# Performance work log

Measured on AMD Instinct MI355X. Metric: run time of the kernel, lower is better.

The kernel has to match this reference:

```python
import jax, jax.numpy as jnp
import numpy as np

B, S, D_IN, UNITS = 4, 4096, 512, 128

def setup_inputs() -> dict:
    key = jax.random.key(0)
    k_in, k_wq, k_wk, k_wv = jax.random.split(key, 4)
    scale = 1.0 / np.sqrt(D_IN)
    return {
        "inputs": jax.random.normal(k_in, (B, S, D_IN), dtype=jnp.float32),
        "Wq": jax.random.normal(k_wq, (D_IN, UNITS), dtype=jnp.float32) * scale,
        "bq": jnp.zeros((UNITS,), dtype=jnp.float32),
        "Wk": jax.random.normal(k_wk, (D_IN, UNITS), dtype=jnp.float32) * scale,
        "bk": jnp.zeros((UNITS,), dtype=jnp.float32),
        "Wv": jax.random.normal(k_wv, (D_IN, UNITS), dtype=jnp.float32) * scale,
        "bv": jnp.zeros((UNITS,), dtype=jnp.float32),
    }

def reference(inputs, Wq, bq, Wk, bk, Wv, bv):
    # Dense + ReLU projections (Keras Dense default has bias)
    q = jax.nn.relu(jnp.einsum('bsd,du->bsu', inputs, Wq) + bq)  # [B,S,U]
    k = jax.nn.relu(jnp.einsum('bsd,du->bsu', inputs, Wk) + bk)
    v = jax.nn.relu(jnp.einsum('bsd,du->bsu', inputs, Wv) + bv)
    # Raw (unscaled) attention: softmax(Q K^T) V
    scores = jnp.einsum('bsu,btu->bst', q, k)                    # [B,S,S]
    attn = jax.nn.softmax(scores, axis=-1)
    return jnp.einsum('bst,btu->bsu', attn, v)                   # [B,S,U]
```

## Files before the change

kernel.cpp:

```cpp
#include <hip/hip_runtime.h>
#include <stdint.h>

#define Bq 4
#define Sq 4096
#define DIN 512
#define Uq 128
#define Mq (Bq * Sq)
#define LOG2E 1.44269504f

typedef __attribute__((ext_vector_type(8))) _Float16 f16x8;
typedef __attribute__((ext_vector_type(4))) float f32x4;
typedef unsigned short u16;

__device__ __forceinline__ u16 f2h(float f) {
  union { _Float16 h; u16 u; } v;
  v.h = (_Float16)f;
  return v.u;
}
__device__ __forceinline__ unsigned pk2(float a, float b) {
  return __builtin_bit_cast(unsigned, __builtin_amdgcn_cvt_pkrtz(a, b));
}
__device__ __forceinline__ void gl_lds16(const void* g, void* l) {
  __builtin_amdgcn_global_load_lds(
      (const __attribute__((address_space(1))) unsigned int*)g,
      (__attribute__((address_space(3))) unsigned int*)l, 16, 0, 0);
}

__global__ __launch_bounds__(256) void wt_kernel(const float* __restrict__ Wqp,
                                                 const float* __restrict__ Wkp,
                                                 const float* __restrict__ Wvp,
                                                 u16* __restrict__ wt) {
  int idx = blockIdx.x * 256 + threadIdx.x;
  int z = idx >> 16, r = idx & 65535;
  int n = r >> 9, k = r & 511;
  const float* W = (z == 0) ? Wqp : ((z == 1) ? Wkp : Wvp);
  wt[idx] = f2h(W[k * Uq + n]);
}

__global__ __launch_bounds__(256, 2) void proj_kernel(const float* __restrict__ X,
                                                      const u16* __restrict__ Wt,
                                                      const float* __restrict__ bqp,
                                                      const float* __restrict__ bkp,
                                                      const float* __restrict__ bvp,
                                                      u16* __restrict__ qkv) {
  const int mbase = blockIdx.x * 32;
  const int tid = threadIdx.x;
  const int wid = tid >> 6, lane = tid & 63;
  const int lo = lane & 15, g = lane >> 4;

  __shared__ __align__(16) u16 xt[32][40];

  f32x4 acc[2][6];
#pragma unroll
  for (int mg = 0; mg < 2; ++mg)
#pragma unroll
    for (int fi = 0; fi < 6; ++fi) acc[mg][fi] = (f32x4){0.f, 0.f, 0.f, 0.f};

  const int xrow = tid >> 2, xcc = (tid & 3) * 8;
  const float* xsrc = X + (size_t)(mbase + xrow) * DIN + xcc;
  float4 nv0, nv1;
  if (tid < 128) {
    nv0 = *(const float4*)xsrc;
    nv1 = *(const float4*)(xsrc + 4);
  }

  const u16* wp[6];
#pragma unroll
  for (int fi = 0; fi < 6; ++fi) {
    const int gf = 6 * wid + fi;
    const int R = (gf >> 3) * 128 + (gf & 7) * 16 + lo;
    wp[fi] = Wt + (size_t)R * 512 + 8 * g;
  }
  f16x8 bw[6];
#pragma unroll
  for (int fi = 0; fi < 6; ++fi) bw[fi] = *(const f16x8*)(wp[fi]);

  for (int step = 0; step < 16; ++step) {
    if (tid < 128) {
      union { u16 u[8]; uint4 v; } pk;
      pk.u[0] = f2h(nv0.x); pk.u[1] = f2h(nv0.y); pk.u[2] = f2h(nv0.z); pk.u[3] = f2h(nv0.w);
      pk.u[4] = f2h(nv1.x); pk.u[5] = f2h(nv1.y); pk.u[6] = f2h(nv1.z); pk.u[7] = f2h(nv1.w);
      *(uint4*)(&xt[xrow][xcc]) = pk.v;
    }
    __syncthreads();
    if (step < 15 && tid < 128) {
      const float* s2 = xsrc + (step + 1) * 32;
      nv0 = *(const float4*)s2;
      nv1 = *(const float4*)(s2 + 4);
    }
    f16x8 a0 = *(const f16x8*)(&xt[lo][8 * g]);
    f16x8 a1 = *(const f16x8*)(&xt[16 + lo][8 * g]);
#pragma unroll
    for (int fi = 0; fi < 6; ++fi) {
      acc[0][fi] = __builtin_amdgcn_mfma_f32_16x16x32_f16(a0, bw[fi], acc[0][fi], 0, 0, 0);
      acc[1][fi] = __builtin_amdgcn_mfma_f32_16x16x32_f16(a1, bw[fi], acc[1][fi], 0, 0, 0);
    }
    if (step < 15) {
#pragma unroll
      for (int fi = 0; fi < 6; ++fi)
        bw[fi] = *(const f16x8*)(wp[fi] + (step + 1) * 32);
    }
    __syncthreads();
  }

#pragma unroll
  for (int fi = 0; fi < 6; ++fi) {
    const int gf = 6 * wid + fi;
    const int z = gf >> 3, fl = gf & 7;
    const float* bias = (z == 0) ? bqp : ((z == 1) ? bkp : bvp);
    const float bb = bias[fl * 16 + lo];
    if (z < 2) {
      u16* dst = qkv + (size_t)z * Mq * Uq;
      const float qs = (z == 0) ? LOG2E : 1.0f;
#pragma unroll
      for (int mg = 0; mg < 2; ++mg)
#pragma unroll
        for (int r = 0; r < 4; ++r) {
          const int m = mbase + 16 * mg + 4 * g + r;
          dst[(size_t)m * Uq + fl * 16 + lo] = f2h(fmaxf(acc[mg][fi][r] + bb, 0.f) * qs);
        }
    } else {
      u16* vT = qkv + (size_t)2 * Mq * Uq;
      const int n = fl * 16 + lo;
#pragma unroll
      for (int mg = 0; mg < 2; ++mg) {
        const int m0 = mbase + 16 * mg + 4 * g;
        const int bb_ = m0 >> 12, s0 = m0 & (Sq - 1);
        ushort4 pv = make_ushort4(f2h(fmaxf(acc[mg][fi][0] + bb, 0.f)),
                                  f2h(fmaxf(acc[mg][fi][1] + bb, 0.f)),
                                  f2h(fmaxf(acc[mg][fi][2] + bb, 0.f)),
                                  f2h(fmaxf(acc[mg][fi][3] + bb, 0.f)));
        *(ushort4*)(vT + (size_t)bb_ * Uq * Sq + (size_t)n * Sq + s0) = pv;
      }
    }
  }
}

__global__ __launch_bounds__(256, 3) void attn_kernel(const u16* __restrict__ qkv,
                                                      float* __restrict__ op,
                                                      float2* __restrict__ mlp,
                                                      int kvlen) {
  const int nb = gridDim.x;
  const int bid = blockIdx.x;
  const int xcd = bid & 7, idx = bid >> 3;
  const int b = xcd >> 1;
  const int within = (xcd & 1) * (nb >> 3) + idx;
  const int split = within >> 6, qblk = within & 63;
  const int kv0 = split * kvlen;
  const int nit = kvlen >> 6;

  const int tid = threadIdx.x;
  const int wid = tid >> 6, lane = tid & 63;
  const int lo = lane & 15, g = lane >> 4;

  const u16* kbase = qkv + (size_t)Mq * Uq + (size_t)b * Sq * Uq;
  const u16* vbase = qkv + (size_t)2 * Mq * Uq + (size_t)b * Uq * Sq;

  __shared__ __align__(16) unsigned char kt[16384];
  __shared__ __align__(16) unsigned char vt[16384];
  __shared__ __align__(16) unsigned char plds[4][2048];

  const int s4 = lane >> 4, j16 = lane & 15;
  const char* kg = (const char*)kbase + (size_t)(kv0 + 16 * wid) * 256 + 16 * lane;
  const int kwo0 = (16 * wid + 0 + s4) * 256 + ((j16 ^ ((0 + s4) & 7)) << 4);
  const int kwo1 = (16 * wid + 4 + s4) * 256 + ((j16 ^ ((4 + s4) & 7)) << 4);
  const int kwo2 = (16 * wid + 8 + s4) * 256 + ((j16 ^ ((8 + s4) & 7)) << 4);
  const int kwo3 = (16 * wid + 12 + s4) * 256 + ((j16 ^ ((12 + s4) & 7)) << 4);

  const int s8 = lane >> 3, j8 = lane & 7;
  const int vo = s8 * 8192 + ((j8 ^ s8) << 4);
  const char* vgp = (const char*)vbase + (size_t)kv0 * 2 + (size_t)wid * 262144 + vo;
  char* vl = (char*)vt + wid * 4096;

#define VSTAGE() do {                       \
    gl_lds16(vgp,          vl);             \
    gl_lds16(vgp + 65536,  vl + 1024);      \
    gl_lds16(vgp + 131072, vl + 2048);      \
    gl_lds16(vgp + 196608, vl + 3072);      \
  } while (0)

  const int qrow = b * Sq + qblk * 64 + wid * 16 + lo;
  f16x8 qf[4];
#pragma unroll
  for (int t = 0; t < 4; ++t)
    qf[t] = *(const f16x8*)(qkv + (size_t)qrow * Uq + 32 * t + 8 * g);

  char* const pl = (char*)plds;
  const int pbase = wid * 2048 + lo * 128;
  const int pw0 = pbase + (((g >> 1) ^ (lo & 7)) << 4) + 8 * (g & 1);
  const int pr0 = pbase + ((g ^ (lo & 7)) << 4);

  f32x4 acc[8];
#pragma unroll
  for (int f = 0; f < 8; ++f) acc[f] = (f32x4){0.f, 0.f, 0.f, 0.f};
  float m_run = -1e30f, l_run = 0.f;

  VSTAGE();
  uint4 ka0 = *(const uint4*)(kg + 0);
  uint4 ka1 = *(const uint4*)(kg + 1024);
  uint4 ka2 = *(const uint4*)(kg + 2048);
  uint4 ka3 = *(const uint4*)(kg + 3072);
  kg += 16384;
  asm volatile("s_waitcnt vmcnt(0)" ::: "memory");
  *(uint4*)(&kt[kwo0]) = ka0;
  *(uint4*)(&kt[kwo1]) = ka1;
  *(uint4*)(&kt[kwo2]) = ka2;
  *(uint4*)(&kt[kwo3]) = ka3;
  if (nit > 1) {
    ka0 = *(const uint4*)(kg + 0);
    ka1 = *(const uint4*)(kg + 1024);
    ka2 = *(const uint4*)(kg + 2048);
    ka3 = *(const uint4*)(kg + 3072);
    kg += 16384;
  }
  asm volatile("s_waitcnt lgkmcnt(0)" ::: "memory");
  __builtin_amdgcn_sched_barrier(0);
  __builtin_amdgcn_s_barrier();
  __builtin_amdgcn_sched_barrier(0);

  for (int it = 0; it < nit; ++it) {
    f32x4 sf[4];
    __builtin_amdgcn_s_setprio(1);
#pragma unroll
    for (int h = 0; h < 4; ++h) {
      sf[h] = (f32x4){0.f, 0.f, 0.f, 0.f};
      const int row = 16 * h + lo;
#pragma unroll
      for (int t = 0; t < 4; ++t) {
        f16x8 a = *(const f16x8*)(&kt[row * 256 + ((64 * t + 16 * g) ^ ((lo & 7) << 4))]);
        sf[h] = __builtin_amdgcn_mfma_f32_16x16x32_f16(a, qf[t], sf[h], 0, 0, 0);
      }
    }
    __builtin_amdgcn_s_setprio(0);

    float tmax = -1e30f;
#pragma unroll
    for (int h = 0; h < 4; ++h)
#pragma unroll
      for (int r = 0; r < 4; ++r) tmax = fmaxf(tmax, sf[h][r]);
    tmax = fmaxf(tmax, __shfl_xor(tmax, 16));
    tmax = fmaxf(tmax, __shfl_xor(tmax, 32));

    if (__any(tmax > m_run + 8.f)) {
      const float m_new = fmaxf(m_run, tmax);
      const float scale = exp2f(m_run - m_new);
#pragma unroll
      for (int r = 0; r < 4; ++r) {
        const float sc = __shfl(scale, 4 * g + r);
#pragma unroll
        for (int f = 0; f < 8; ++f) acc[f][r] *= sc;
      }
      l_run *= scale;
      m_run = m_new;
    }

    float psum = 0.f;
    float p[16];
#pragma unroll
    for (int h = 0; h < 4; ++h)
#pragma unroll
      for (int r = 0; r < 4; ++r) {
        const float pv = exp2f(sf[h][r] - m_run);
        psum += pv;
        p[4 * h + r] = pv;
      }
    psum += __shfl_xor(psum, 16);
    psum += __shfl_xor(psum, 32);
    l_run += psum;

#pragma unroll
    for (int h = 0; h < 4; ++h) {
      uint2 pq = make_uint2(pk2(p[4 * h + 0], p[4 * h + 1]),
                            pk2(p[4 * h + 2], p[4 * h + 3]));
      *(uint2*)(pl + (pw0 ^ (h << 5))) = pq;
    }

    asm volatile("s_waitcnt vmcnt(0)" ::: "memory");
    __builtin_amdgcn_sched_barrier(0);
    __builtin_amdgcn_s_barrier();
    __builtin_amdgcn_sched_barrier(0);

    __builtin_amdgcn_s_setprio(1);
#pragma unroll
    for (int s = 0; s < 2; ++s) {
      f16x8 pa = *(const f16x8*)(pl + (pr0 ^ (s << 6)));
#pragma unroll
      for (int f = 0; f < 8; ++f) {
        const int n = 16 * f + lo;
        f16x8 bv = *(const f16x8*)(&vt[n * 128 + ((64 * s + 16 * g) ^ ((lo & 7) << 4))]);
        acc[f] = __builtin_amdgcn_mfma_f32_16x16x32_f16(pa, bv, acc[f], 0, 0, 0);
      }
    }
    __builtin_amdgcn_s_setprio(0);

    if (it + 1 < nit) {
      *(uint4*)(&kt[kwo0]) = ka0;
      *(uint4*)(&kt[kwo1]) = ka1;
      *(uint4*)(&kt[kwo2]) = ka2;
      *(uint4*)(&kt[kwo3]) = ka3;
    }
    asm volatile("s_waitcnt lgkmcnt(0)" ::: "memory");
    __builtin_amdgcn_sched_barrier(0);
    __builtin_amdgcn_s_barrier();
    __builtin_amdgcn_sched_barrier(0);

    if (it + 1 < nit) {
      vgp += 128;
      VSTAGE();
      if (it + 2 < nit) {
        ka0 = *(const uint4*)(kg + 0);
        ka1 = *(const uint4*)(kg + 1024);
        ka2 = *(const uint4*)(kg + 2048);
        ka3 = *(const uint4*)(kg + 3072);
        kg += 16384;
      }
    }
  }
#undef VSTAGE

  const size_t rb = (size_t)split * Mq + (size_t)b * Sq + qblk * 64 + wid * 16;
  if (g == 0) mlp[rb + lo] = make_float2(m_run, l_run);
  float* od = op + rb * Uq;
#pragma unroll
  for (int f = 0; f < 8; ++f) {
    const int n = 16 * f + lo;
#pragma unroll
    for (int r = 0; r < 4; ++r)
      od[(size_t)(4 * g + r) * Uq + n] = acc[f][r];
  }
}

__global__ __launch_bounds__(256) void combine_kernel(const float* __restrict__ op,
                                                      const float2* __restrict__ mlp,
                                                      float* __restrict__ out,
                                                      int nsplit) {
  const int idx = blockIdx.x * 256 + threadIdx.x;
  const int q = idx >> 5, nq = idx & 31;
  float M = -1e30f;
  for (int s = 0; s < nsplit; ++s) M = fmaxf(M, mlp[(size_t)s * Mq + q].x);
  float L = 0.f;
  float ox = 0.f, oy = 0.f, oz = 0.f, ow = 0.f;
  for (int s = 0; s < nsplit; ++s) {
    const float2 ml = mlp[(size_t)s * Mq + q];
    const float w = exp2f(ml.x - M);
    L += w * ml.y;
    const float4 v = *(const float4*)(op + ((size_t)s * Mq + q) * Uq + nq * 4);
    ox += w * v.x; oy += w * v.y; oz += w * v.z; ow += w * v.w;
  }
  const float inv = 1.f / L;
  *(float4*)(out + (size_t)q * Uq + nq * 4) = make_float4(ox * inv, oy * inv, oz * inv, ow * inv);
}

extern "C" void kernel_launch(void* const* d_in, const int* in_sizes, int n_in,
                              void* d_out, int out_size, void* d_ws, size_t ws_size,
                              hipStream_t stream) {
  const float* X   = (const float*)d_in[0];
  const float* Wqp = (const float*)d_in[1];
  const float* bqp = (const float*)d_in[2];
  const float* Wkp = (const float*)d_in[3];
  const float* bkp = (const float*)d_in[4];
  const float* Wvp = (const float*)d_in[5];
  const float* bvp = (const float*)d_in[6];
  float* out = (float*)d_out;

  u16* qkv = (u16*)d_ws;
  u16* wt  = qkv + (size_t)3 * Mq * Uq;
  float* op = (float*)(wt + 3 * 65536);

  const size_t base = (size_t)12976128;
  const size_t per  = (size_t)8519680;
  int nsplit = 4;
  if (ws_size < base + 4 * per) nsplit = 2;
  if (ws_size < base + 2 * per) nsplit = 1;
  float2* mlp = (float2*)(op + (size_t)nsplit * Mq * Uq);

  wt_kernel<<<768, 256, 0, stream>>>(Wqp, Wkp, Wvp, wt);
  proj_kernel<<<Mq / 32, 256, 0, stream>>>(X, wt, bqp, bkp, bvp, qkv);
  attn_kernel<<<256 * nsplit, 256, 0, stream>>>(qkv, op, mlp, Sq / nsplit);
  combine_kernel<<<(Mq * 32) / 256, 256, 0, stream>>>(op, mlp, out, nsplit);
}
```

Measured before the change: 98.15 us.

## Process two query subtiles per wave to reuse K/V tiles across 128 queries

Each wave now handles 32 query rows (two 16-row subtiles) instead of 16, so each block covers 128 queries and reuses every K and V LDS tile across twice as many MFMAs. The grid is halved, the P buffer doubles, and occupancy hints drop from 3 to 2 blocks per CU to fit the doubled accumulators and scores. This targets K/V load and LDS traffic per unit of compute, at the cost of more registers, fewer resident waves and fewer blocks to spread across CUs.

```diff
diff --git a/kernel.cpp b/kernel.cpp
--- a/kernel.cpp
+++ b/kernel.cpp
@@ -136,7 +136,7 @@
   }
 }
 
-__global__ __launch_bounds__(256, 3) void attn_kernel(const u16* __restrict__ qkv,
+__global__ __launch_bounds__(256, 2) void attn_kernel(const u16* __restrict__ qkv,
                                                       float* __restrict__ op,
                                                       float2* __restrict__ mlp,
                                                       int kvlen) {
@@ -145,7 +145,7 @@
   const int xcd = bid & 7, idx = bid >> 3;
   const int b = xcd >> 1;
   const int within = (xcd & 1) * (nb >> 3) + idx;
-  const int split = within >> 6, qblk = within & 63;
+  const int split = within >> 5, qblk = within & 31;
   const int kv0 = split * kvlen;
   const int nit = kvlen >> 6;
 
@@ -158,7 +158,7 @@
 
   __shared__ __align__(16) unsigned char kt[16384];
   __shared__ __align__(16) unsigned char vt[16384];
-  __shared__ __align__(16) unsigned char plds[4][2048];
+  __shared__ __align__(16) unsigned char plds[4][4096];
 
   const int s4 = lane >> 4, j16 = lane & 15;
   const char* kg = (const char*)kbase + (size_t)(kv0 + 16 * wid) * 256 + 16 * lane;
@@ -179,21 +179,24 @@
     gl_lds16(vgp + 196608, vl + 3072);      \
   } while (0)
 
-  const int qrow = b * Sq + qblk * 64 + wid * 16 + lo;
-  f16x8 qf[4];
-#pragma unroll
-  for (int t = 0; t < 4; ++t)
-    qf[t] = *(const f16x8*)(qkv + (size_t)qrow * Uq + 32 * t + 8 * g);
-
-  char* const pl = (char*)plds;
-  const int pbase = wid * 2048 + lo * 128;
-  const int pw0 = pbase + (((g >> 1) ^ (lo & 7)) << 4) + 8 * (g & 1);
-  const int pr0 = pbase + ((g ^ (lo & 7)) << 4);
-
-  f32x4 acc[8];
-#pragma unroll
-  for (int f = 0; f < 8; ++f) acc[f] = (f32x4){0.f, 0.f, 0.f, 0.f};
-  float m_run = -1e30f, l_run = 0.f;
+  const int qrow0 = b * Sq + qblk * 128 + wid * 32 + lo;
+  f16x8 qf[2][4];
+#pragma unroll
+  for (int sq = 0; sq < 2; ++sq)
+#pragma unroll
+    for (int t = 0; t < 4; ++t)
+      qf[sq][t] = *(const f16x8*)(qkv + (size_t)(qrow0 + 16 * sq) * Uq + 32 * t + 8 * g);
+
+  char* const pl = (char*)plds + wid * 4096;
+  const int pw0 = lo * 128 + (((g >> 1) ^ (lo & 7)) << 4) + 8 * (g & 1);
+  const int pr0 = lo * 128 + ((g ^ (lo & 7)) << 4);
+
+  f32x4 acc[2][8];
+#pragma unroll
+  for (int sq = 0; sq < 2; ++sq)
+#pragma unroll
+    for (int f = 0; f < 8; ++f) acc[sq][f] = (f32x4){0.f, 0.f, 0.f, 0.f};
+  float m_run[2] = {-1e30f, -1e30f}, l_run[2] = {0.f, 0.f};
 
   VSTAGE();
   uint4 ka0 = *(const uint4*)(kg + 0);
@@ -219,60 +222,64 @@
   __builtin_amdgcn_sched_barrier(0);
 
   for (int it = 0; it < nit; ++it) {
-    f32x4 sf[4];
+    f32x4 sf[2][4];
     __builtin_amdgcn_s_setprio(1);
 #pragma unroll
     for (int h = 0; h < 4; ++h) {
-      sf[h] = (f32x4){0.f, 0.f, 0.f, 0.f};
+      sf[0][h] = (f32x4){0.f, 0.f, 0.f, 0.f};
+      sf[1][h] = (f32x4){0.f, 0.f, 0.f, 0.f};
       const int row = 16 * h + lo;
 #pragma unroll
       for (int t = 0; t < 4; ++t) {
         f16x8 a = *(const f16x8*)(&kt[row * 256 + ((64 * t + 16 * g) ^ ((lo & 7) << 4))]);
-        sf[h] = __builtin_amdgcn_mfma_f32_16x16x32_f16(a, qf[t], sf[h], 0, 0, 0);
+        sf[0][h] = __builtin_amdgcn_mfma_f32_16x16x32_f16(a, qf[0][t], sf[0][h], 0, 0, 0);
+        sf[1][h] = __builtin_amdgcn_mfma_f32_16x16x32_f16(a, qf[1][t], sf[1][h], 0, 0, 0);
       }
     }
     __builtin_amdgcn_s_setprio(0);
 
-    float tmax = -1e30f;
-#pragma unroll
-    for (int h = 0; h < 4; ++h)
-#pragma unroll
-      for (int r = 0; r < 4; ++r) tmax = fmaxf(tmax, sf[h][r]);
-    tmax = fmaxf(tmax, __shfl_xor(tmax, 16));
-    tmax = fmaxf(tmax, __shfl_xor(tmax, 32));
-
-    if (__any(tmax > m_run + 8.f)) {
-      const float m_new = fmaxf(m_run, tmax);
-      const float scale = exp2f(m_run - m_new);
-#pragma unroll
-      for (int r = 0; r < 4; ++r) {
-        const float sc = __shfl(scale, 4 * g + r);
-#pragma unroll
-        for (int f = 0; f < 8; ++f) acc[f][r] *= sc;
-      }
-      l_run *= scale;
-      m_run = m_new;
-    }
-
-    float psum = 0.f;
-    float p[16];
-#pragma unroll
-    for (int h = 0; h < 4; ++h)
-#pragma unroll
-      for (int r = 0; r < 4; ++r) {
-        const float pv = exp2f(sf[h][r] - m_run);
-        psum += pv;
-        p[4 * h + r] = pv;
-      }
-    psum += __shfl_xor(psum, 16);
-    psum += __shfl_xor(psum, 32);
-    l_run += psum;
-
-#pragma unroll
-    for (int h = 0; h < 4; ++h) {
-      uint2 pq = make_uint2(pk2(p[4 * h + 0], p[4 * h + 1]),
-                            pk2(p[4 * h + 2], p[4 * h + 3]));
-      *(uint2*)(pl + (pw0 ^ (h << 5))) = pq;
+#pragma unroll
+    for (int sq = 0; sq < 2; ++sq) {
+      float tmax = -1e30f;
+#pragma unroll
+      for (int h = 0; h < 4; ++h)
+#pragma unroll
+        for (int r = 0; r < 4; ++r) tmax = fmaxf(tmax, sf[sq][h][r]);
+      tmax = fmaxf(tmax, __shfl_xor(tmax, 16));
+      tmax = fmaxf(tmax, __shfl_xor(tmax, 32));
+
+      if (__any(tmax > m_run[sq] + 8.f)) {
+        const float m_new = fmaxf(m_run[sq], tmax);
+        const float scale = exp2f(m_run[sq] - m_new);
+#pragma unroll
+        for (int r = 0; r < 4; ++r) {
+          const float sc = __shfl(scale, 4 * g + r);
+#pragma unroll
+          for (int f = 0; f < 8; ++f) acc[sq][f][r] *= sc;
+        }
+        l_run[sq] *= scale;
+        m_run[sq] = m_new;
+      }
+
+      float psum = 0.f;
+#pragma unroll
+      for (int h = 0; h < 4; ++h)
+#pragma unroll
+        for (int r = 0; r < 4; ++r) {
+          const float pv = exp2f(sf[sq][h][r] - m_run[sq]);
+          psum += pv;
+          sf[sq][h][r] = pv;
+        }
+      psum += __shfl_xor(psum, 16);
+      psum += __shfl_xor(psum, 32);
+      l_run[sq] += psum;
+
+#pragma unroll
+      for (int h = 0; h < 4; ++h) {
+        uint2 pq = make_uint2(pk2(sf[sq][h][0], sf[sq][h][1]),
+                              pk2(sf[sq][h][2], sf[sq][h][3]));
+        *(uint2*)(pl + sq * 2048 + (pw0 ^ (h << 5))) = pq;
+      }
     }
 
     asm volatile("s_waitcnt vmcnt(0)" ::: "memory");
@@ -282,13 +289,15 @@
 
     __builtin_amdgcn_s_setprio(1);
 #pragma unroll
-    for (int s = 0; s < 2; ++s) {
-      f16x8 pa = *(const f16x8*)(pl + (pr0 ^ (s << 6)));
+    for (int ks = 0; ks < 2; ++ks) {
+      f16x8 pa0 = *(const f16x8*)(pl + (pr0 ^ (ks << 6)));
+      f16x8 pa1 = *(const f16x8*)(pl + 2048 + (pr0 ^ (ks << 6)));
 #pragma unroll
       for (int f = 0; f < 8; ++f) {
         const int n = 16 * f + lo;
-        f16x8 bv = *(const f16x8*)(&vt[n * 128 + ((64 * s + 16 * g) ^ ((lo & 7) << 4))]);
-        acc[f] = __builtin_amdgcn_mfma_f32_16x16x32_f16(pa, bv, acc[f], 0, 0, 0);
+        f16x8 bv = *(const f16x8*)(&vt[n * 128 + ((64 * ks + 16 * g) ^ ((lo & 7) << 4))]);
+        acc[0][f] = __builtin_amdgcn_mfma_f32_16x16x32_f16(pa0, bv, acc[0][f], 0, 0, 0);
+        acc[1][f] = __builtin_amdgcn_mfma_f32_16x16x32_f16(pa1, bv, acc[1][f], 0, 0, 0);
       }
     }
     __builtin_amdgcn_s_setprio(0);
@@ -318,15 +327,18 @@
   }
 #undef VSTAGE
 
-  const size_t rb = (size_t)split * Mq + (size_t)b * Sq + qblk * 64 + wid * 16;
-  if (g == 0) mlp[rb + lo] = make_float2(m_run, l_run);
-  float* od = op + rb * Uq;
-#pragma unroll
-  for (int f = 0; f < 8; ++f) {
-    const int n = 16 * f + lo;
-#pragma unroll
-    for (int r = 0; r < 4; ++r)
-      od[(size_t)(4 * g + r) * Uq + n] = acc[f][r];
+#pragma unroll
+  for (int sq = 0; sq < 2; ++sq) {
+    const size_t rb = (size_t)split * Mq + (size_t)b * Sq + qblk * 128 + wid * 32 + sq * 16;
+    if (g == 0) mlp[rb + lo] = make_float2(m_run[sq], l_run[sq]);
+    float* od = op + rb * Uq;
+#pragma unroll
+    for (int f = 0; f < 8; ++f) {
+      const int n = 16 * f + lo;
+#pragma unroll
+      for (int r = 0; r < 4; ++r)
+        od[(size_t)(4 * g + r) * Uq + n] = acc[sq][f][r];
+    }
   }
 }
 
@@ -376,6 +388,6 @@
 
   wt_kernel<<<768, 256, 0, stream>>>(Wqp, Wkp, Wvp, wt);
   proj_kernel<<<Mq / 32, 256, 0, stream>>>(X, wt, bqp, bkp, bvp, qkv);
-  attn_kernel<<<256 * nsplit, 256, 0, stream>>>(qkv, op, mlp, Sq / nsplit);
+  attn_kernel<<<128 * nsplit, 256, 0, stream>>>(qkv, op, mlp, Sq / nsplit);
   combine_kernel<<<(Mq * 32) / 256, 256, 0, stream>>>(op, mlp, out, nsplit);
 }
```

Result: no change. 98.03 us (-0.1%).

## Double-buffer K/V tiles and overlap next QK^T with softmax in attention

Applied to the files above, without the earlier changes.

Turns the attention loop into a two-stage software pipeline. K and V LDS tiles are double-buffered, and the QK^T MFMAs for the next tile are issued before the softmax and PV of the current tile. One barrier per iteration is dropped, and the global waits use partial vmcnt so loads can stay in flight. Doubling LDS and live score registers lowers occupancy to 2 blocks per CU, and the KV split count drops from 4 to 2, giving fewer blocks and less combine work.

```diff
diff --git a/kernel.cpp b/kernel.cpp
--- a/kernel.cpp
+++ b/kernel.cpp
@@ -136,7 +136,7 @@
   }
 }
 
-__global__ __launch_bounds__(256, 3) void attn_kernel(const u16* __restrict__ qkv,
+__global__ __launch_bounds__(256, 2) void attn_kernel(const u16* __restrict__ qkv,
                                                       float* __restrict__ op,
                                                       float2* __restrict__ mlp,
                                                       int kvlen) {
@@ -156,8 +156,8 @@
   const u16* kbase = qkv + (size_t)Mq * Uq + (size_t)b * Sq * Uq;
   const u16* vbase = qkv + (size_t)2 * Mq * Uq + (size_t)b * Uq * Sq;
 
-  __shared__ __align__(16) unsigned char kt[16384];
-  __shared__ __align__(16) unsigned char vt[16384];
+  __shared__ __align__(16) unsigned char kt[2][16384];
+  __shared__ __align__(16) unsigned char vt[2][16384];
   __shared__ __align__(16) unsigned char plds[4][2048];
 
   const int s4 = lane >> 4, j16 = lane & 15;
@@ -170,13 +170,41 @@
   const int s8 = lane >> 3, j8 = lane & 7;
   const int vo = s8 * 8192 + ((j8 ^ s8) << 4);
   const char* vgp = (const char*)vbase + (size_t)kv0 * 2 + (size_t)wid * 262144 + vo;
-  char* vl = (char*)vt + wid * 4096;
-
-#define VSTAGE() do {                       \
-    gl_lds16(vgp,          vl);             \
-    gl_lds16(vgp + 65536,  vl + 1024);      \
-    gl_lds16(vgp + 131072, vl + 2048);      \
-    gl_lds16(vgp + 196608, vl + 3072);      \
+
+#define VSTAGE(BUF) do {                                    \
+    char* vl = (char*)&vt[BUF][wid * 4096];                 \
+    gl_lds16(vgp,          vl);                             \
+    gl_lds16(vgp + 65536,  vl + 1024);                      \
+    gl_lds16(vgp + 131072, vl + 2048);                      \
+    gl_lds16(vgp + 196608, vl + 3072);                      \
+  } while (0)
+
+#define KLOAD() do {                                        \
+    ka0 = *(const uint4*)(kg + 0);                          \
+    ka1 = *(const uint4*)(kg + 1024);                       \
+    ka2 = *(const uint4*)(kg + 2048);                       \
+    ka3 = *(const uint4*)(kg + 3072);                       \
+    kg += 16384;                                            \
+  } while (0)
+
+#define KWRITE(BUF) do {                                    \
+    *(uint4*)(&kt[BUF][kwo0]) = ka0;                        \
+    *(uint4*)(&kt[BUF][kwo1]) = ka1;                        \
+    *(uint4*)(&kt[BUF][kwo2]) = ka2;                        \
+    *(uint4*)(&kt[BUF][kwo3]) = ka3;                        \
+  } while (0)
+
+#define QKBLOCK(BUF, SD) do {                               \
+    _Pragma("unroll")                                       \
+    for (int h = 0; h < 4; ++h) {                           \
+      SD[h] = (f32x4){0.f, 0.f, 0.f, 0.f};                  \
+      const int row_ = 16 * h + lo;                         \
+      _Pragma("unroll")                                     \
+      for (int t = 0; t < 4; ++t) {                         \
+        f16x8 a_ = *(const f16x8*)(&kt[BUF][row_ * 256 + ((64 * t + 16 * g) ^ ((lo & 7) << 4))]); \
+        SD[h] = __builtin_amdgcn_mfma_f32_16x16x32_f16(a_, qf[t], SD[h], 0, 0, 0); \
+      }                                                     \
+    }                                                       \
   } while (0)
 
   const int qrow = b * Sq + qblk * 64 + wid * 16 + lo;
@@ -185,137 +213,109 @@
   for (int t = 0; t < 4; ++t)
     qf[t] = *(const f16x8*)(qkv + (size_t)qrow * Uq + 32 * t + 8 * g);
 
-  char* const pl = (char*)plds;
-  const int pbase = wid * 2048 + lo * 128;
-  const int pw0 = pbase + (((g >> 1) ^ (lo & 7)) << 4) + 8 * (g & 1);
-  const int pr0 = pbase + ((g ^ (lo & 7)) << 4);
+  char* const pl = (char*)plds + wid * 2048;
+  const int pw0 = lo * 128 + (((g >> 1) ^ (lo & 7)) << 4) + 8 * (g & 1);
+  const int pr0 = lo * 128 + ((g ^ (lo & 7)) << 4);
 
   f32x4 acc[8];
 #pragma unroll
   for (int f = 0; f < 8; ++f) acc[f] = (f32x4){0.f, 0.f, 0.f, 0.f};
   float m_run = -1e30f, l_run = 0.f;
 
-  VSTAGE();
-  uint4 ka0 = *(const uint4*)(kg + 0);
-  uint4 ka1 = *(const uint4*)(kg + 1024);
-  uint4 ka2 = *(const uint4*)(kg + 2048);
-  uint4 ka3 = *(const uint4*)(kg + 3072);
-  kg += 16384;
-  asm volatile("s_waitcnt vmcnt(0)" ::: "memory");
-  *(uint4*)(&kt[kwo0]) = ka0;
-  *(uint4*)(&kt[kwo1]) = ka1;
-  *(uint4*)(&kt[kwo2]) = ka2;
-  *(uint4*)(&kt[kwo3]) = ka3;
-  if (nit > 1) {
-    ka0 = *(const uint4*)(kg + 0);
-    ka1 = *(const uint4*)(kg + 1024);
-    ka2 = *(const uint4*)(kg + 2048);
-    ka3 = *(const uint4*)(kg + 3072);
-    kg += 16384;
-  }
+  uint4 ka0, ka1, ka2, ka3;
+
+  VSTAGE(0); vgp += 128;
+  VSTAGE(1); vgp += 128;
+  KLOAD(); KWRITE(0);
+  KLOAD(); KWRITE(1);
+  if (nit > 2) KLOAD();
   asm volatile("s_waitcnt lgkmcnt(0)" ::: "memory");
   __builtin_amdgcn_sched_barrier(0);
   __builtin_amdgcn_s_barrier();
   __builtin_amdgcn_sched_barrier(0);
 
-  for (int it = 0; it < nit; ++it) {
-    f32x4 sf[4];
-    __builtin_amdgcn_s_setprio(1);
-#pragma unroll
-    for (int h = 0; h < 4; ++h) {
-      sf[h] = (f32x4){0.f, 0.f, 0.f, 0.f};
-      const int row = 16 * h + lo;
-#pragma unroll
-      for (int t = 0; t < 4; ++t) {
-        f16x8 a = *(const f16x8*)(&kt[row * 256 + ((64 * t + 16 * g) ^ ((lo & 7) << 4))]);
-        sf[h] = __builtin_amdgcn_mfma_f32_16x16x32_f16(a, qf[t], sf[h], 0, 0, 0);
-      }
-    }
-    __builtin_amdgcn_s_setprio(0);
-
-    float tmax = -1e30f;
-#pragma unroll
-    for (int h = 0; h < 4; ++h)
-#pragma unroll
-      for (int r = 0; r < 4; ++r) tmax = fmaxf(tmax, sf[h][r]);
-    tmax = fmaxf(tmax, __shfl_xor(tmax, 16));
-    tmax = fmaxf(tmax, __shfl_xor(tmax, 32));
-
-    if (__any(tmax > m_run + 8.f)) {
-      const float m_new = fmaxf(m_run, tmax);
-      const float scale = exp2f(m_run - m_new);
-#pragma unroll
-      for (int r = 0; r < 4; ++r) {
-        const float sc = __shfl(scale, 4 * g + r);
-#pragma unroll
-        for (int f = 0; f < 8; ++f) acc[f][r] *= sc;
-      }
-      l_run *= scale;
-      m_run = m_new;
-    }
-
-    float psum = 0.f;
-    float p[16];
-#pragma unroll
-    for (int h = 0; h < 4; ++h)
-#pragma unroll
-      for (int r = 0; r < 4; ++r) {
-        const float pv = exp2f(sf[h][r] - m_run);
-        psum += pv;
-        p[4 * h + r] = pv;
-      }
-    psum += __shfl_xor(psum, 16);
-    psum += __shfl_xor(psum, 32);
-    l_run += psum;
-
-#pragma unroll
-    for (int h = 0; h < 4; ++h) {
-      uint2 pq = make_uint2(pk2(p[4 * h + 0], p[4 * h + 1]),
-                            pk2(p[4 * h + 2], p[4 * h + 3]));
-      *(uint2*)(pl + (pw0 ^ (h << 5))) = pq;
-    }
-
-    asm volatile("s_waitcnt vmcnt(0)" ::: "memory");
-    __builtin_amdgcn_sched_barrier(0);
-    __builtin_amdgcn_s_barrier();
-    __builtin_amdgcn_sched_barrier(0);
-
-    __builtin_amdgcn_s_setprio(1);
-#pragma unroll
-    for (int s = 0; s < 2; ++s) {
-      f16x8 pa = *(const f16x8*)(pl + (pr0 ^ (s << 6)));
-#pragma unroll
-      for (int f = 0; f < 8; ++f) {
-        const int n = 16 * f + lo;
-        f16x8 bv = *(const f16x8*)(&vt[n * 128 + ((64 * s + 16 * g) ^ ((lo & 7) << 4))]);
-        acc[f] = __builtin_amdgcn_mfma_f32_16x16x32_f16(pa, bv, acc[f], 0, 0, 0);
-      }
-    }
-    __builtin_amdgcn_s_setprio(0);
-
-    if (it + 1 < nit) {
-      *(uint4*)(&kt[kwo0]) = ka0;
-      *(uint4*)(&kt[kwo1]) = ka1;
-      *(uint4*)(&kt[kwo2]) = ka2;
-      *(uint4*)(&kt[kwo3]) = ka3;
-    }
-    asm volatile("s_waitcnt lgkmcnt(0)" ::: "memory");
-    __builtin_amdgcn_sched_barrier(0);
-    __builtin_amdgcn_s_barrier();
-    __builtin_amdgcn_sched_barrier(0);
-
-    if (it + 1 < nit) {
-      vgp += 128;
-      VSTAGE();
-      if (it + 2 < nit) {
-        ka0 = *(const uint4*)(kg + 0);
-        ka1 = *(const uint4*)(kg + 1024);
-        ka2 = *(const uint4*)(kg + 2048);
-        ka3 = *(const uint4*)(kg + 3072);
-        kg += 16384;
-      }
-    }
-  }
+  f32x4 sfA[4], sfB[4];
+  QKBLOCK(0, sfA);
+
+#define AITER(IT, PAR, SC, SN) do {                                            \
+                \
+    __builtin_amdgcn_s_setprio(1);                                             \
+    if ((IT) + 1 < nit) QKBLOCK((PAR) ^ 1, SN);                                \
+    __builtin_amdgcn_s_setprio(0);                                             \
+    if ((IT) + 2 < nit) KWRITE(PAR);              \
+    float tmax = -1e30f;                                                       \
+    _Pragma("unroll")                                                          \
+    for (int h = 0; h < 4; ++h)                                                \
+      _Pragma("unroll")                                                        \
+      for (int r = 0; r < 4; ++r) tmax = fmaxf(tmax, SC[h][r]);                \
+    tmax = fmaxf(tmax, __shfl_xor(tmax, 16));                                  \
+    tmax = fmaxf(tmax, __shfl_xor(tmax, 32));                                  \
+    if (__any(tmax > m_run + 8.f)) {                                           \
+      const float m_new = fmaxf(m_run, tmax);                                  \
+      const float scale = exp2f(m_run - m_new);                                \
+      _Pragma("unroll")                                                        \
+      for (int r = 0; r < 4; ++r) {                                            \
+        const float sc_ = __shfl(scale, 4 * g + r);                            \
+        _Pragma("unroll")                                                      \
+        for (int f = 0; f < 8; ++f) acc[f][r] *= sc_;                          \
+      }                                                                        \
+      l_run *= scale;                                                          \
+      m_run = m_new;                                                           \
+    }                                                                          \
+    float psum = 0.f;                                                          \
+    _Pragma("unroll")                                                          \
+    for (int h = 0; h < 4; ++h)                                                \
+      _Pragma("unroll")                                                        \
+      for (int r = 0; r < 4; ++r) {                                            \
+        const float pv_ = exp2f(SC[h][r] - m_run);                             \
+        psum += pv_;                                                           \
+        SC[h][r] = pv_;                                                        \
+      }                                                                        \
+    psum += __shfl_xor(psum, 16);                                              \
+    psum += __shfl_xor(psum, 32);                                              \
+    l_run += psum;                                                             \
+    _Pragma("unroll")                                                          \
+    for (int h = 0; h < 4; ++h) {                                              \
+      uint2 pq_ = make_uint2(pk2(SC[h][0], SC[h][1]), pk2(SC[h][2], SC[h][3]));\
+      *(uint2*)(pl + (pw0 ^ (h << 5))) = pq_;                                  \
+    }                                                                          \
+                     \
+    __builtin_amdgcn_s_setprio(1);                                             \
+    _Pragma("unroll")                                                          \
+    for (int ks = 0; ks < 2; ++ks) {                                           \
+      f16x8 pa_ = *(const f16x8*)(pl + (pr0 ^ (ks << 6)));                     \
+      _Pragma("unroll")                                                        \
+      for (int f = 0; f < 8; ++f) {                                            \
+        const int n_ = 16 * f + lo;                                            \
+        f16x8 bv_ = *(const f16x8*)(&vt[PAR][n_ * 128 + ((64 * ks + 16 * g) ^ ((lo & 7) << 4))]); \
+        acc[f] = __builtin_amdgcn_mfma_f32_16x16x32_f16(pa_, bv_, acc[f], 0, 0, 0); \
+      }                                                                        \
+    }                                                                          \
+    __builtin_amdgcn_s_setprio(0);                                             \
+    __builtin_amdgcn_sched_barrier(0);                                         \
+    __builtin_amdgcn_s_barrier();         \
+    __builtin_amdgcn_sched_barrier(0);                                         \
+    if ((IT) + 3 < nit) KLOAD();                          \
+    __builtin_amdgcn_sched_barrier(0);                                         \
+    if ((IT) + 2 < nit) { VSTAGE(PAR); vgp += 128; }   \
+    __builtin_amdgcn_sched_barrier(0);                                         \
+    if ((IT) + 3 < nit)      asm volatile("s_waitcnt vmcnt(8)" ::: "memory");  \
+    else if ((IT) + 2 < nit) asm volatile("s_waitcnt vmcnt(4)" ::: "memory");  \
+    else                     asm volatile("s_waitcnt vmcnt(0)" ::: "memory");  \
+    asm volatile("s_waitcnt lgkmcnt(0)" ::: "memory");                         \
+    __builtin_amdgcn_sched_barrier(0);                                         \
+    __builtin_amdgcn_s_barrier();           \
+    __builtin_amdgcn_sched_barrier(0);                                         \
+  } while (0)
+
+  for (int it = 0; it < nit; it += 2) {
+    AITER(it,     0, sfA, sfB);
+    AITER(it + 1, 1, sfB, sfA);
+  }
+#undef AITER
+#undef QKBLOCK
+#undef KWRITE
+#undef KLOAD
 #undef VSTAGE
 
   const size_t rb = (size_t)split * Mq + (size_t)b * Sq + qblk * 64 + wid * 16;
@@ -369,8 +369,7 @@
 
   const size_t base = (size_t)12976128;
   const size_t per  = (size_t)8519680;
-  int nsplit = 4;
-  if (ws_size < base + 4 * per) nsplit = 2;
+  int nsplit = 2;
   if (ws_size < base + 2 * per) nsplit = 1;
   float2* mlp = (float2*)(op + (size_t)nsplit * Mq * Uq);
 
```

Result: slower. 106.3 us (+8.3%).

## Switch attention kernel to 32x32x16 MFMA with 128-row query blocks

Applied to the files above, without the earlier changes.

The attention kernel moves from 16x16x32 to 32x32x16 f16 MFMA tiles. Each wave now owns 32 query rows, so each block covers 128 queries and the grid is halved. This gives twice the K/V reuse per LDS load and fewer MFMA issues per FLOP. In exchange the P staging buffer doubles, rescale factors go through a small LDS array, register pressure rises (launch bounds go from 3 to 2 blocks per CU), and fewer blocks are available to fill the GPU.

```diff
diff --git a/kernel.cpp b/kernel.cpp
--- a/kernel.cpp
+++ b/kernel.cpp
@@ -10,6 +10,7 @@
 
 typedef __attribute__((ext_vector_type(8))) _Float16 f16x8;
 typedef __attribute__((ext_vector_type(4))) float f32x4;
+typedef __attribute__((ext_vector_type(16))) float f32x16;
 typedef unsigned short u16;
 
 __device__ __forceinline__ u16 f2h(float f) {
@@ -25,6 +26,8 @@
       (const __attribute__((address_space(1))) unsigned int*)g,
       (__attribute__((address_space(3))) unsigned int*)l, 16, 0, 0);
 }
+__device__ __forceinline__ float xmax32(float v) { return fmaxf(v, __shfl_xor(v, 32)); }
+__device__ __forceinline__ float xsum32(float v) { return v + __shfl_xor(v, 32); }
 
 __global__ __launch_bounds__(256) void wt_kernel(const float* __restrict__ Wqp,
                                                  const float* __restrict__ Wkp,
@@ -136,7 +139,7 @@
   }
 }
 
-__global__ __launch_bounds__(256, 3) void attn_kernel(const u16* __restrict__ qkv,
+__global__ __launch_bounds__(256, 2) void attn_kernel(const u16* __restrict__ qkv,
                                                       float* __restrict__ op,
                                                       float2* __restrict__ mlp,
                                                       int kvlen) {
@@ -145,20 +148,21 @@
   const int xcd = bid & 7, idx = bid >> 3;
   const int b = xcd >> 1;
   const int within = (xcd & 1) * (nb >> 3) + idx;
-  const int split = within >> 6, qblk = within & 63;
+  const int split = within >> 5, qblk = within & 31;
   const int kv0 = split * kvlen;
   const int nit = kvlen >> 6;
 
   const int tid = threadIdx.x;
   const int wid = tid >> 6, lane = tid & 63;
-  const int lo = lane & 15, g = lane >> 4;
+  const int l32 = lane & 31, hi = lane >> 5;
 
   const u16* kbase = qkv + (size_t)Mq * Uq + (size_t)b * Sq * Uq;
   const u16* vbase = qkv + (size_t)2 * Mq * Uq + (size_t)b * Uq * Sq;
 
   __shared__ __align__(16) unsigned char kt[16384];
   __shared__ __align__(16) unsigned char vt[16384];
-  __shared__ __align__(16) unsigned char plds[4][2048];
+  __shared__ __align__(16) unsigned char plds[4][4096];
+  __shared__ float smx[4][32];
 
   const int s4 = lane >> 4, j16 = lane & 15;
   const char* kg = (const char*)kbase + (size_t)(kv0 + 16 * wid) * 256 + 16 * lane;
@@ -170,7 +174,7 @@
   const int s8 = lane >> 3, j8 = lane & 7;
   const int vo = s8 * 8192 + ((j8 ^ s8) << 4);
   const char* vgp = (const char*)vbase + (size_t)kv0 * 2 + (size_t)wid * 262144 + vo;
-  char* vl = (char*)vt + wid * 4096;
+  char* const vl = (char*)vt + wid * 4096;
 
 #define VSTAGE() do {                       \
     gl_lds16(vgp,          vl);             \
@@ -178,102 +182,117 @@
     gl_lds16(vgp + 131072, vl + 2048);      \
     gl_lds16(vgp + 196608, vl + 3072);      \
   } while (0)
-
-  const int qrow = b * Sq + qblk * 64 + wid * 16 + lo;
-  f16x8 qf[4];
-#pragma unroll
-  for (int t = 0; t < 4; ++t)
-    qf[t] = *(const f16x8*)(qkv + (size_t)qrow * Uq + 32 * t + 8 * g);
-
-  char* const pl = (char*)plds;
-  const int pbase = wid * 2048 + lo * 128;
-  const int pw0 = pbase + (((g >> 1) ^ (lo & 7)) << 4) + 8 * (g & 1);
-  const int pr0 = pbase + ((g ^ (lo & 7)) << 4);
-
-  f32x4 acc[8];
-#pragma unroll
-  for (int f = 0; f < 8; ++f) acc[f] = (f32x4){0.f, 0.f, 0.f, 0.f};
+#define KLOAD() do {                        \
+    ka0 = *(const uint4*)(kg + 0);          \
+    ka1 = *(const uint4*)(kg + 1024);       \
+    ka2 = *(const uint4*)(kg + 2048);       \
+    ka3 = *(const uint4*)(kg + 3072);       \
+    kg += 16384;                            \
+  } while (0)
+#define KWRITE() do {                       \
+    *(uint4*)(&kt[kwo0]) = ka0;             \
+    *(uint4*)(&kt[kwo1]) = ka1;             \
+    *(uint4*)(&kt[kwo2]) = ka2;             \
+    *(uint4*)(&kt[kwo3]) = ka3;             \
+  } while (0)
+
+  const int qrow = b * Sq + qblk * 128 + wid * 32 + l32;
+  f16x8 qf[8];
+#pragma unroll
+  for (int ks = 0; ks < 8; ++ks)
+    qf[ks] = *(const f16x8*)(qkv + (size_t)qrow * Uq + 16 * ks + 8 * hi);
+
+  f32x16 acc4[4];
+#pragma unroll
+  for (int f = 0; f < 4; ++f) acc4[f] = (f32x16){};
   float m_run = -1e30f, l_run = 0.f;
+  float* const smxw = &smx[wid][0];
+
+  const int q7 = l32 & 7;
+  char* const plw = (char*)plds + wid * 4096 + l32 * 128 + 8 * hi;
+  const char* const plr = (const char*)plds + wid * 4096 + l32 * 128;
+
+  uint4 ka0, ka1, ka2, ka3;
 
   VSTAGE();
-  uint4 ka0 = *(const uint4*)(kg + 0);
-  uint4 ka1 = *(const uint4*)(kg + 1024);
-  uint4 ka2 = *(const uint4*)(kg + 2048);
-  uint4 ka3 = *(const uint4*)(kg + 3072);
-  kg += 16384;
+  KLOAD();
   asm volatile("s_waitcnt vmcnt(0)" ::: "memory");
-  *(uint4*)(&kt[kwo0]) = ka0;
-  *(uint4*)(&kt[kwo1]) = ka1;
-  *(uint4*)(&kt[kwo2]) = ka2;
-  *(uint4*)(&kt[kwo3]) = ka3;
-  if (nit > 1) {
-    ka0 = *(const uint4*)(kg + 0);
-    ka1 = *(const uint4*)(kg + 1024);
-    ka2 = *(const uint4*)(kg + 2048);
-    ka3 = *(const uint4*)(kg + 3072);
-    kg += 16384;
-  }
+  KWRITE();
+  if (nit > 1) KLOAD();
   asm volatile("s_waitcnt lgkmcnt(0)" ::: "memory");
   __builtin_amdgcn_sched_barrier(0);
   __builtin_amdgcn_s_barrier();
   __builtin_amdgcn_sched_barrier(0);
 
   for (int it = 0; it < nit; ++it) {
-    f32x4 sf[4];
+    f32x16 sf0 = (f32x16){}, sf1 = (f32x16){};
     __builtin_amdgcn_s_setprio(1);
 #pragma unroll
-    for (int h = 0; h < 4; ++h) {
-      sf[h] = (f32x4){0.f, 0.f, 0.f, 0.f};
-      const int row = 16 * h + lo;
-#pragma unroll
-      for (int t = 0; t < 4; ++t) {
-        f16x8 a = *(const f16x8*)(&kt[row * 256 + ((64 * t + 16 * g) ^ ((lo & 7) << 4))]);
-        sf[h] = __builtin_amdgcn_mfma_f32_16x16x32_f16(a, qf[t], sf[h], 0, 0, 0);
-      }
+    for (int ks = 0; ks < 8; ++ks) {
+      const int co = ((2 * ks + hi) ^ q7) << 4;
+      f16x8 a0 = *(const f16x8*)(&kt[l32 * 256 + co]);
+      f16x8 a1 = *(const f16x8*)(&kt[(32 + l32) * 256 + co]);
+      sf0 = __builtin_amdgcn_mfma_f32_32x32x16_f16(a0, qf[ks], sf0, 0, 0, 0);
+      sf1 = __builtin_amdgcn_mfma_f32_32x32x16_f16(a1, qf[ks], sf1, 0, 0, 0);
     }
     __builtin_amdgcn_s_setprio(0);
 
-    float tmax = -1e30f;
-#pragma unroll
-    for (int h = 0; h < 4; ++h)
-#pragma unroll
-      for (int r = 0; r < 4; ++r) tmax = fmaxf(tmax, sf[h][r]);
-    tmax = fmaxf(tmax, __shfl_xor(tmax, 16));
-    tmax = fmaxf(tmax, __shfl_xor(tmax, 32));
+    float t8[8];
+#pragma unroll
+    for (int i = 0; i < 8; ++i)
+      t8[i] = fmaxf(fmaxf(sf0[i], sf0[i + 8]), fmaxf(sf1[i], sf1[i + 8]));
+#pragma unroll
+    for (int i = 0; i < 4; ++i) t8[i] = fmaxf(t8[i], t8[i + 4]);
+    float tmax = fmaxf(fmaxf(t8[0], t8[1]), fmaxf(t8[2], t8[3]));
+    tmax = xmax32(tmax);
 
     if (__any(tmax > m_run + 8.f)) {
       const float m_new = fmaxf(m_run, tmax);
-      const float scale = exp2f(m_run - m_new);
-#pragma unroll
-      for (int r = 0; r < 4; ++r) {
-        const float sc = __shfl(scale, 4 * g + r);
-#pragma unroll
-        for (int f = 0; f < 8; ++f) acc[f][r] *= sc;
-      }
-      l_run *= scale;
+      const float sc = exp2f(m_run - m_new);
+      if (lane < 32) smxw[l32] = sc;
+#pragma unroll
+      for (int r = 0; r < 16; ++r) {
+        const float scr = smxw[(r & 3) + 8 * (r >> 2) + 4 * hi];
+#pragma unroll
+        for (int f = 0; f < 4; ++f) acc4[f][r] *= scr;
+      }
+      l_run *= sc;
       m_run = m_new;
     }
 
     float psum = 0.f;
-    float p[16];
-#pragma unroll
-    for (int h = 0; h < 4; ++h)
-#pragma unroll
-      for (int r = 0; r < 4; ++r) {
-        const float pv = exp2f(sf[h][r] - m_run);
-        psum += pv;
-        p[4 * h + r] = pv;
-      }
-    psum += __shfl_xor(psum, 16);
-    psum += __shfl_xor(psum, 32);
-    l_run += psum;
-
-#pragma unroll
-    for (int h = 0; h < 4; ++h) {
-      uint2 pq = make_uint2(pk2(p[4 * h + 0], p[4 * h + 1]),
-                            pk2(p[4 * h + 2], p[4 * h + 3]));
-      *(uint2*)(pl + (pw0 ^ (h << 5))) = pq;
-    }
+    unsigned Ap[2][4], Bp[2][4];
+#pragma unroll
+    for (int ks2 = 0; ks2 < 2; ++ks2) {
+#pragma unroll
+      for (int m = 0; m < 4; ++m) {
+        const float s0v = ks2 ? sf1[4 * m + 0] : sf0[4 * m + 0];
+        const float s1v = ks2 ? sf1[4 * m + 1] : sf0[4 * m + 1];
+        const float s2v = ks2 ? sf1[4 * m + 2] : sf0[4 * m + 2];
+        const float s3v = ks2 ? sf1[4 * m + 3] : sf0[4 * m + 3];
+        const float p0 = exp2f(s0v - m_run), p1 = exp2f(s1v - m_run);
+        const float p2 = exp2f(s2v - m_run), p3 = exp2f(s3v - m_run);
+        psum += (p0 + p1) + (p2 + p3);
+        Ap[ks2][m] = pk2(p0, p1);
+        Bp[ks2][m] = pk2(p2, p3);
+      }
+    }
+    l_run += xsum32(psum);
+
+#pragma unroll
+    for (int ks2 = 0; ks2 < 2; ++ks2)
+#pragma unroll
+      for (int m = 0; m < 4; ++m) {
+        const int c = 4 * ks2 + m;
+        *(uint2*)(plw + ((c ^ q7) << 4)) = make_uint2(Ap[ks2][m], Bp[ks2][m]);
+      }
+    f16x8 pa[4];
+#pragma unroll
+    for (int ks2 = 0; ks2 < 2; ++ks2)
+#pragma unroll
+      for (int kk = 0; kk < 2; ++kk)
+        pa[2 * ks2 + kk] =
+            *(const f16x8*)(plr + (((4 * ks2 + 2 * kk + hi) ^ q7) << 4));
 
     asm volatile("s_waitcnt vmcnt(0)" ::: "memory");
     __builtin_amdgcn_sched_barrier(0);
@@ -282,23 +301,17 @@
 
     __builtin_amdgcn_s_setprio(1);
 #pragma unroll
-    for (int s = 0; s < 2; ++s) {
-      f16x8 pa = *(const f16x8*)(pl + (pr0 ^ (s << 6)));
-#pragma unroll
-      for (int f = 0; f < 8; ++f) {
-        const int n = 16 * f + lo;
-        f16x8 bv = *(const f16x8*)(&vt[n * 128 + ((64 * s + 16 * g) ^ ((lo & 7) << 4))]);
-        acc[f] = __builtin_amdgcn_mfma_f32_16x16x32_f16(pa, bv, acc[f], 0, 0, 0);
+    for (int ks = 0; ks < 4; ++ks) {
+#pragma unroll
+      for (int f = 0; f < 4; ++f) {
+        const int d = 32 * f + l32;
+        f16x8 bv = *(const f16x8*)(&vt[d * 128 + (((2 * ks + hi) ^ q7) << 4)]);
+        acc4[f] = __builtin_amdgcn_mfma_f32_32x32x16_f16(pa[ks], bv, acc4[f], 0, 0, 0);
       }
     }
     __builtin_amdgcn_s_setprio(0);
 
-    if (it + 1 < nit) {
-      *(uint4*)(&kt[kwo0]) = ka0;
-      *(uint4*)(&kt[kwo1]) = ka1;
-      *(uint4*)(&kt[kwo2]) = ka2;
-      *(uint4*)(&kt[kwo3]) = ka3;
-    }
+    if (it + 1 < nit) KWRITE();
     asm volatile("s_waitcnt lgkmcnt(0)" ::: "memory");
     __builtin_amdgcn_sched_barrier(0);
     __builtin_amdgcn_s_barrier();
@@ -307,27 +320,23 @@
     if (it + 1 < nit) {
       vgp += 128;
       VSTAGE();
-      if (it + 2 < nit) {
-        ka0 = *(const uint4*)(kg + 0);
-        ka1 = *(const uint4*)(kg + 1024);
-        ka2 = *(const uint4*)(kg + 2048);
-        ka3 = *(const uint4*)(kg + 3072);
-        kg += 16384;
-      }
+      if (it + 2 < nit) KLOAD();
     }
   }
 #undef VSTAGE
-
-  const size_t rb = (size_t)split * Mq + (size_t)b * Sq + qblk * 64 + wid * 16;
-  if (g == 0) mlp[rb + lo] = make_float2(m_run, l_run);
+#undef KLOAD
+#undef KWRITE
+
+  const size_t rb = (size_t)split * Mq + (size_t)b * Sq + qblk * 128 + wid * 32;
+  if (lane < 32) mlp[rb + lane] = make_float2(m_run, l_run);
   float* od = op + rb * Uq;
 #pragma unroll
-  for (int f = 0; f < 8; ++f) {
-    const int n = 16 * f + lo;
-#pragma unroll
-    for (int r = 0; r < 4; ++r)
-      od[(size_t)(4 * g + r) * Uq + n] = acc[f][r];
-  }
+  for (int f = 0; f < 4; ++f)
+#pragma unroll
+    for (int r = 0; r < 16; ++r) {
+      const int qr = (r & 3) + 8 * (r >> 2) + 4 * hi;
+      od[(size_t)qr * Uq + 32 * f + l32] = acc4[f][r];
+    }
 }
 
 __global__ __launch_bounds__(256) void combine_kernel(const float* __restrict__ op,
@@ -376,6 +385,6 @@
 
   wt_kernel<<<768, 256, 0, stream>>>(Wqp, Wkp, Wvp, wt);
   proj_kernel<<<Mq / 32, 256, 0, stream>>>(X, wt, bqp, bkp, bvp, qkv);
-  attn_kernel<<<256 * nsplit, 256, 0, stream>>>(qkv, op, mlp, Sq / nsplit);
+  attn_kernel<<<128 * nsplit, 256, 0, stream>>>(qkv, op, mlp, Sq / nsplit);
   combine_kernel<<<(Mq * 32) / 256, 256, 0, stream>>>(op, mlp, out, nsplit);
 }
```

Measured after the change: 94.46 us. 3.8% less time.
